# Optimization experiments

Measured on AMD Instinct MI355X. Metric: run time of the kernel, lower is better.

Reference implementation:

```python
import jax, jax.numpy as jnp
import numpy as np
from jax import lax

B, NPG = 128, 1024          # graphs, nodes per graph
N = B * NPG                  # total nodes
AVG_DEG = 8
E = N * AVG_DEG              # total edges
F_N, F_E = 128, 32           # node / edge feature dims
LATENT = [32, 32, 32, 1]
D = sum(LATENT)              # total_latent_dim = 97
K = 30                       # sort-pooling k
C1, C2, KW2 = 16, 32, 5      # conv1d channels / kernel
OUT = 2
DENSE = ((K - 2) // 2 + 1 - KW2 + 1) * C2  # 352


def setup_inputs() -> dict:
    key = jax.random.key(0)
    ks = jax.random.split(key, 12)
    inp = {}
    inp["node_feat"] = jax.random.normal(ks[0], (N, F_N), jnp.float32)
    inp["edge_feat"] = jax.random.normal(ks[1], (E, F_E), jnp.float32)
    inp["edge_index"] = jax.random.randint(ks[2], (2, E), 0, N)
    dims = [F_N + F_E] + LATENT
    for i in range(4):
        inp[f"W{i}"] = jax.random.normal(ks[3 + i], (dims[i], dims[i + 1]), jnp.float32) * 0.05
        inp[f"b{i}"] = jnp.zeros((dims[i + 1],), jnp.float32)
    inp["w_conv1"] = jax.random.normal(ks[7], (C1, 1, D), jnp.float32) * 0.05
    inp["b_conv1"] = jnp.zeros((C1,), jnp.float32)
    inp["w_conv2"] = jax.random.normal(ks[8], (C2, C1, KW2), jnp.float32) * 0.05
    inp["b_conv2"] = jnp.zeros((C2,), jnp.float32)
    inp["w_out"] = jax.random.normal(ks[9], (DENSE, OUT), jnp.float32) * 0.05
    inp["b_out"] = jnp.zeros((OUT,), jnp.float32)
    return inp


def _maxpool2(x):
    # MaxPool1d(2, 2) over last axis of [B, C, L]
    return lax.reduce_window(x, -jnp.inf, lax.max, (1, 1, 2), (1, 1, 2), "VALID")


def _forward(node_feat, edge_feat, W0, b0, W1, b1, W2, b2, W3, b3,
             w_conv1, b_conv1, w_conv2, b_conv2, w_out, b_out, edge_index):
    src, dst = edge_index[0], edge_index[1]
    # degree with self-loop, as in DGCNN (divide by deg after linear)
    deg = jnp.ones((N,), node_feat.dtype).at[dst].add(1.0)
    # e2npool: sum incident edge features onto destination nodes
    e2n = jax.ops.segment_sum(edge_feat, dst, num_segments=N)
    cur = jnp.concatenate([node_feat, e2n], axis=1)  # [N, F_N+F_E]
    hops = []
    for W, b in ((W0, b0), (W1, b1), (W2, b2), (W3, b3)):
        # (A + I) X  -> Linear -> / deg -> tanh
        pooled = jax.ops.segment_sum(cur[src], dst, num_segments=N) + cur
        cur = jnp.tanh((pooled @ W + b) / deg[:, None])
        hops.append(cur)
    feat = jnp.concatenate(hops, axis=1).reshape(B, NPG, D)  # [B, NPG, 97]
    # SortPooling: top-k nodes per graph by last latent channel
    _, idx = lax.top_k(feat[:, :, -1], K)                    # [B, K]
    sp = jnp.take_along_axis(feat, idx[:, :, None], axis=1)  # [B, K, D]
    x = sp.reshape(B, 1, K * D)
    x = lax.conv_general_dilated(x, w_conv1, (D,), "VALID",
                                 dimension_numbers=("NCH", "OIH", "NCH"))
    x = jax.nn.relu(x + b_conv1[None, :, None])  # [B, 16, 30]
    x = _maxpool2(x)                              # [B, 16, 15]
    x = lax.conv_general_dilated(x, w_conv2, (1,), "VALID",
                                 dimension_numbers=("NCH", "OIH", "NCH"))
    x = jax.nn.relu(x + b_conv2[None, :, None])  # [B, 32, 11]
    x = x.reshape(B, -1)                          # [B, 352]
    return jax.nn.relu(x @ w_out + b_out)         # [B, OUT]


def reference(node_feat, edge_feat, edge_index, W0, b0, W1, b1, W2, b2, W3, b3,
              w_conv1, b_conv1, w_conv2, b_conv2, w_out, b_out):
    return _forward(node_feat, edge_feat, W0, b0, W1, b1, W2, b2, W3, b3,
                    w_conv1, b_conv1, w_conv2, b_conv2, w_out, b_out, edge_index)
```

## Files before the change

kernel.cpp:

```cpp
#include <hip/hip_runtime.h>
#include <hip/hip_bf16.h>
#include <math.h>

#define N_NODES 131072
#define N_EDGES 1048576
#define B_GR    128
#define NPG_    1024
#define KTOP    30


__global__ __launch_bounds__(256) void k_zero(int* cnt) {
    int i = blockIdx.x * 256 + threadIdx.x;
    if (i < N_NODES) cnt[i] = 0;
}

__global__ __launch_bounds__(256) void k_count(const int* __restrict__ dst, int* __restrict__ cnt) {
    int xcd = blockIdx.x & 7;
    int base = (blockIdx.x >> 3) * 4096 + threadIdx.x;
    #pragma unroll
    for (int it = 0; it < 16; ++it) {
        int e = base + it * 256;
        int d = __builtin_nontemporal_load(dst + e);
        if ((d >> 14) == xcd) atomicAdd(&cnt[d], 1);
    }
}

__global__ __launch_bounds__(256) void k_scan1(const int* __restrict__ cnt,
                                               int* __restrict__ row_start,
                                               int* __restrict__ blocksum) {
    __shared__ int s[256];
    int t = threadIdx.x;
    int i = blockIdx.x * 256 + t;
    int v = cnt[i];
    s[t] = v; __syncthreads();
    for (int o = 1; o < 256; o <<= 1) {
        int x = (t >= o) ? s[t - o] : 0;
        __syncthreads();
        s[t] += x;
        __syncthreads();
    }
    row_start[i] = s[t] - v;
    if (t == 255) blocksum[blockIdx.x] = s[t];
}

__global__ __launch_bounds__(512) void k_scan2(int* __restrict__ blocksum) {
    __shared__ int s[512];
    int t = threadIdx.x;
    int v = blocksum[t];
    s[t] = v; __syncthreads();
    for (int o = 1; o < 512; o <<= 1) {
        int x = (t >= o) ? s[t - o] : 0;
        __syncthreads();
        s[t] += x;
        __syncthreads();
    }
    blocksum[t] = s[t] - v;
}

__global__ __launch_bounds__(256) void k_scan3(int* __restrict__ row_start,
                                               const int* __restrict__ blocksum,
                                               int* __restrict__ cursor) {
    int i = blockIdx.x * 256 + threadIdx.x;
    int r = row_start[i] + blocksum[blockIdx.x];
    row_start[i] = r;
    cursor[i] = r;
}

__global__ __launch_bounds__(256) void k_fill(const int* __restrict__ src,
                                              const int* __restrict__ dst,
                                              int* __restrict__ cursor,
                                              int* __restrict__ csr_src,
                                              int* __restrict__ csr_eid) {
    int xcd = blockIdx.x & 7;
    int base = (blockIdx.x >> 3) * 4096 + threadIdx.x;
    #pragma unroll
    for (int it = 0; it < 16; ++it) {
        int e = base + it * 256;
        int d = __builtin_nontemporal_load(dst + e);
        if ((d >> 14) == xcd) {
            int s = __builtin_nontemporal_load(src + e);
            int pos = atomicAdd(&cursor[d], 1);
            csr_src[pos] = s;
            csr_eid[pos] = e;
        }
    }
}


__global__ __launch_bounds__(256) void k_esum(const float* __restrict__ ef,
                                              const int* __restrict__ row_start,
                                              const int* __restrict__ cnt,
                                              const int* __restrict__ csr_eid,
                                              float* __restrict__ esum) {
    int g = threadIdx.x >> 5, j = threadIdx.x & 31;
    int n0 = (blockIdx.x * 8 + g) * 4;
    int st[4], ln[4];
    #pragma unroll
    for (int i = 0; i < 4; ++i) { st[i] = row_start[n0 + i]; ln[i] = cnt[n0 + i]; }
    float acc[4] = {0.f, 0.f, 0.f, 0.f};
    int base = 0;
    while ((ln[0] > base) | (ln[1] > base) | (ln[2] > base) | (ln[3] > base)) {
        int eid[4][8];
        #pragma unroll
        for (int i = 0; i < 4; ++i) {
            #pragma unroll
            for (int s = 0; s < 8; ++s) {
                int idx = base + s;
                int a = st[i] + ((idx < ln[i]) ? idx : 0);
                a = (a < N_EDGES) ? a : 0;
                eid[i][s] = csr_eid[a];
            }
        }
        #pragma unroll
        for (int i = 0; i < 4; ++i) {
            #pragma unroll
            for (int s = 0; s < 8; ++s) {
                float v = ef[(size_t)eid[i][s] * 32 + j];
                acc[i] += ((base + s) < ln[i]) ? v : 0.f;
            }
        }
        base += 8;
    }
    #pragma unroll
    for (int i = 0; i < 4; ++i)
        esum[(size_t)(n0 + i) * 32 + j] = acc[i];
}


__global__ __launch_bounds__(256) void k_gemm160(const float* __restrict__ nf,
                                                 const float* __restrict__ esum,
                                                 const float* __restrict__ W0,
                                                 float* __restrict__ z0) {
    __shared__ float a[64 * 161];
    int tid = threadIdx.x;
    int n0 = blockIdx.x * 64;
    const float* nfb = nf + (size_t)n0 * 128;
    for (int f = tid; f < 8192; f += 256) {
        int n = f >> 7, k = f & 127;
        a[n * 161 + k] = nfb[f];
    }
    const float* esb = esum + (size_t)n0 * 32;
    for (int f = tid; f < 2048; f += 256) {
        int n = f >> 5, k = f & 31;
        a[n * 161 + 128 + k] = esb[f];
    }
    __syncthreads();
    int wv = __builtin_amdgcn_readfirstlane(tid >> 6);
    int lane = tid & 63;
    int c0 = wv * 8;
    float acc[8] = {0.f, 0.f, 0.f, 0.f, 0.f, 0.f, 0.f, 0.f};
    const float* ar = a + lane * 161;
    for (int k = 0; k < 160; ++k) {
        float av = ar[k];
        #pragma unroll
        for (int jj = 0; jj < 8; ++jj)
            acc[jj] += av * W0[k * 32 + c0 + jj];
    }
    float* zr = z0 + (size_t)(n0 + lane) * 32 + c0;
    *(float4*)zr = make_float4(acc[0], acc[1], acc[2], acc[3]);
    *(float4*)(zr + 4) = make_float4(acc[4], acc[5], acc[6], acc[7]);
}


__global__ __launch_bounds__(256) void k_layer(const float* __restrict__ zin,
                                               const int* __restrict__ row_start,
                                               const int* __restrict__ cnt,
                                               const int* __restrict__ csr_src,
                                               const float* __restrict__ bias,
                                               const float* __restrict__ Wn,
                                               float* __restrict__ hout,
                                               float* __restrict__ znext) {
    __shared__ float Ws[1024];
    int tid = threadIdx.x;
    for (int f = tid; f < 1024; f += 256) Ws[f] = Wn[f];
    __syncthreads();
    int g = tid >> 5, j = tid & 31;
    int n0 = (blockIdx.x * 8 + g) * 4;
    int st[4], ln[4];
    #pragma unroll
    for (int i = 0; i < 4; ++i) { st[i] = row_start[n0 + i]; ln[i] = cnt[n0 + i]; }
    float acc[4];
    #pragma unroll
    for (int i = 0; i < 4; ++i) acc[i] = zin[(size_t)(n0 + i) * 32 + j];
    int base = 0;
    while ((ln[0] > base) | (ln[1] > base) | (ln[2] > base) | (ln[3] > base)) {
        int sid[4][8];
        #pragma unroll
        for (int i = 0; i < 4; ++i) {
            #pragma unroll
            for (int s = 0; s < 8; ++s) {
                int idx = base + s;
                int a = st[i] + ((idx < ln[i]) ? idx : 0);
                a = (a < N_EDGES) ? a : 0;
                sid[i][s] = csr_src[a];
            }
        }
        #pragma unroll
        for (int i = 0; i < 4; ++i) {
            #pragma unroll
            for (int s = 0; s < 8; ++s) {
                float v = zin[(size_t)sid[i][s] * 32 + j];
                acc[i] += ((base + s) < ln[i]) ? v : 0.f;
            }
        }
        base += 8;
    }
    float bj = bias[j];
    float h[4];
    #pragma unroll
    for (int i = 0; i < 4; ++i) {
        float deg = 1.f + (float)ln[i];
        h[i] = tanhf((acc[i] + bj) / deg);
        hout[(size_t)(n0 + i) * 32 + j] = h[i];
    }
    float z[4] = {0.f, 0.f, 0.f, 0.f};
    for (int k = 0; k < 32; ++k) {
        float w = Ws[k * 32 + j];
        #pragma unroll
        for (int i = 0; i < 4; ++i)
            z[i] += __shfl(h[i], k, 32) * w;
    }
    #pragma unroll
    for (int i = 0; i < 4; ++i)
        znext[(size_t)(n0 + i) * 32 + j] = z[i];
}


__global__ __launch_bounds__(256) void k_layer3(const float* __restrict__ zin,
                                                const int* __restrict__ row_start,
                                                const int* __restrict__ cnt,
                                                const int* __restrict__ csr_src,
                                                const float* __restrict__ bias,
                                                const float* __restrict__ W3,
                                                float* __restrict__ hout,
                                                float* __restrict__ z3) {
    int g = threadIdx.x >> 5, j = threadIdx.x & 31;
    int n0 = (blockIdx.x * 8 + g) * 4;
    int st[4], ln[4];
    #pragma unroll
    for (int i = 0; i < 4; ++i) { st[i] = row_start[n0 + i]; ln[i] = cnt[n0 + i]; }
    float acc[4];
    #pragma unroll
    for (int i = 0; i < 4; ++i) acc[i] = zin[(size_t)(n0 + i) * 32 + j];
    int base = 0;
    while ((ln[0] > base) | (ln[1] > base) | (ln[2] > base) | (ln[3] > base)) {
        int sid[4][8];
        #pragma unroll
        for (int i = 0; i < 4; ++i) {
            #pragma unroll
            for (int s = 0; s < 8; ++s) {
                int idx = base + s;
                int a = st[i] + ((idx < ln[i]) ? idx : 0);
                a = (a < N_EDGES) ? a : 0;
                sid[i][s] = csr_src[a];
            }
        }
        #pragma unroll
        for (int i = 0; i < 4; ++i) {
            #pragma unroll
            for (int s = 0; s < 8; ++s) {
                float v = zin[(size_t)sid[i][s] * 32 + j];
                acc[i] += ((base + s) < ln[i]) ? v : 0.f;
            }
        }
        base += 8;
    }
    float bj = bias[j];
    float w3 = W3[j];
    #pragma unroll
    for (int i = 0; i < 4; ++i) {
        float deg = 1.f + (float)ln[i];
        float h = tanhf((acc[i] + bj) / deg);
        hout[(size_t)(n0 + i) * 32 + j] = h;
        float t = h * w3;
        #pragma unroll
        for (int o = 16; o; o >>= 1) t += __shfl_xor(t, o, 32);
        if (j == 0) z3[n0 + i] = t;
    }
}


__global__ __launch_bounds__(256) void k_g3(const float* __restrict__ z3,
                                            const int* __restrict__ row_start,
                                            const int* __restrict__ cnt,
                                            const int* __restrict__ csr_src,
                                            const float* __restrict__ b3,
                                            float* __restrict__ val) {
    int n = blockIdx.x * 256 + threadIdx.x;
    int start = row_start[n], len = cnt[n];
    const int* cs = csr_src + start;
    float s = z3[n];
    int i = 0;
    for (; i + 4 <= len; i += 4)
        s += z3[cs[i]] + z3[cs[i + 1]] + z3[cs[i + 2]] + z3[cs[i + 3]];
    for (; i < len; ++i) s += z3[cs[i]];
    float deg = 1.f + (float)len;
    val[n] = tanhf((s + b3[0]) / deg);
}


__global__ __launch_bounds__(256) void k_head(const float* __restrict__ h0,
                                              const float* __restrict__ h1,
                                              const float* __restrict__ h2,
                                              const float* __restrict__ val,
                                              const float* __restrict__ wc1,
                                              const float* __restrict__ bc1,
                                              const float* __restrict__ wc2,
                                              const float* __restrict__ bc2,
                                              const float* __restrict__ wout,
                                              const float* __restrict__ bout,
                                              float* __restrict__ out) {
    __shared__ float vals[1024];
    __shared__ int selidx[KTOP];
    __shared__ float sp[KTOP * 97];
    __shared__ float y1[16 * 30];
    __shared__ float pool[16 * 15];
    __shared__ float y2[352];
    int b = blockIdx.x, tid = threadIdx.x;
    const float* vb = val + (size_t)b * NPG_;
    for (int u = tid; u < NPG_; u += 256) vals[u] = vb[u];
    __syncthreads();
    if (tid < 64) {
        unsigned long long keys[16];
        #pragma unroll
        for (int r = 0; r < 16; ++r) {
            int u = tid * 16 + r;
            unsigned int bb = __float_as_uint(vals[u]);
            unsigned int ord = (bb & 0x80000000u) ? ~bb : (bb | 0x80000000u);
            keys[r] = ((unsigned long long)ord << 32) |
                      (unsigned long long)(0xFFFFFFFFu - (unsigned int)u);
        }
        for (int k = 0; k < KTOP; ++k) {
            unsigned long long m = keys[0];
            #pragma unroll
            for (int r = 1; r < 16; ++r) m = (keys[r] > m) ? keys[r] : m;
            #pragma unroll
            for (int o = 32; o; o >>= 1) {
                unsigned long long t = __shfl_xor(m, o);
                m = (t > m) ? t : m;
            }
            int u = (int)(0xFFFFFFFFu - (unsigned int)(m & 0xFFFFFFFFull));
            if (tid == 0) selidx[k] = u;
            #pragma unroll
            for (int r = 0; r < 16; ++r)
                if (tid * 16 + r == u) keys[r] = 0ull;
        }
    }
    __syncthreads();
    size_t nb = (size_t)b * NPG_;
    for (int idx = tid; idx < KTOP * 32; idx += 256) {
        int t = idx >> 5, d = idx & 31;
        size_t s = (nb + (size_t)selidx[t]) * 32;
        sp[t * 97 + d]      = h0[s + d];
        sp[t * 97 + 32 + d] = h1[s + d];
        sp[t * 97 + 64 + d] = h2[s + d];
    }
    if (tid < KTOP) sp[tid * 97 + 96] = vb[selidx[tid]];
    __syncthreads();
    for (int idx = tid; idx < 480; idx += 256) {
        int t = idx >> 4, c = idx & 15;
        float acc = bc1[c];
        for (int d = 0; d < 97; ++d) acc += sp[t * 97 + d] * wc1[c * 97 + d];
        y1[c * 30 + t] = fmaxf(acc, 0.f);
    }
    __syncthreads();
    for (int idx = tid; idx < 240; idx += 256) {
        int c = idx / 15, u = idx - c * 15;
        pool[c * 15 + u] = fmaxf(y1[c * 30 + 2 * u], y1[c * 30 + 2 * u + 1]);
    }
    __syncthreads();
    for (int idx = tid; idx < 352; idx += 256) {
        int o = idx / 11, t = idx - o * 11;
        float acc = bc2[o];
        for (int i = 0; i < 16; ++i)
            for (int kk = 0; kk < 5; ++kk)
                acc += pool[i * 15 + t + kk] * wc2[(o * 16 + i) * 5 + kk];
        y2[idx] = fmaxf(acc, 0.f);
    }
    __syncthreads();
    if (tid < 2) {
        float acc = bout[tid];
        for (int m = 0; m < 352; ++m) acc += y2[m] * wout[m * 2 + tid];
        out[b * 2 + tid] = fmaxf(acc, 0.f);
    }
}


extern "C" void kernel_launch(void* const* d_in, const int* in_sizes, int n_in,
                              void* d_out, int out_size, void* d_ws, size_t ws_size,
                              hipStream_t stream) {
    const float* node_feat = (const float*)d_in[0];
    const float* edge_feat = (const float*)d_in[1];
    const int*   eidx      = (const int*)d_in[2];
    const float* W0 = (const float*)d_in[3];
    const float* b0 = (const float*)d_in[4];
    const float* W1 = (const float*)d_in[5];
    const float* b1 = (const float*)d_in[6];
    const float* W2 = (const float*)d_in[7];
    const float* b2 = (const float*)d_in[8];
    const float* W3 = (const float*)d_in[9];
    const float* b3 = (const float*)d_in[10];
    const float* wc1 = (const float*)d_in[11];
    const float* bc1 = (const float*)d_in[12];
    const float* wc2 = (const float*)d_in[13];
    const float* bc2 = (const float*)d_in[14];
    const float* wout = (const float*)d_in[15];
    const float* bout = (const float*)d_in[16];
    float* out = (float*)d_out;

    const int* src = eidx;
    const int* dst = eidx + N_EDGES;

    char* ws = (char*)d_ws;
    size_t off = 0;
    auto alloc = [&](size_t bytes) -> char* {
        char* p = ws + off;
        off += (bytes + 255) & ~(size_t)255;
        return p;
    };
    int* cnt       = (int*)alloc((size_t)N_NODES * 4);
    int* row_start = (int*)alloc((size_t)N_NODES * 4);
    int* cursor    = (int*)alloc((size_t)N_NODES * 4);
    int* blocksum  = (int*)alloc(512 * 4);
    int* csr_src   = (int*)alloc((size_t)N_EDGES * 4);
    int* csr_eid   = (int*)alloc((size_t)N_EDGES * 4);
    float* esum    = (float*)alloc((size_t)N_NODES * 32 * 4);
    float* z0      = (float*)alloc((size_t)N_NODES * 32 * 4);
    float* z1      = (float*)alloc((size_t)N_NODES * 32 * 4);
    float* z2      = (float*)alloc((size_t)N_NODES * 32 * 4);
    float* h0      = (float*)alloc((size_t)N_NODES * 32 * 4);
    float* h1      = (float*)alloc((size_t)N_NODES * 32 * 4);
    float* h2      = (float*)alloc((size_t)N_NODES * 32 * 4);
    float* z3      = (float*)alloc((size_t)N_NODES * 4);
    float* val     = (float*)alloc((size_t)N_NODES * 4);
    (void)ws_size;

    k_zero<<<N_NODES / 256, 256, 0, stream>>>(cnt);
    k_count<<<2048, 256, 0, stream>>>(dst, cnt);
    k_scan1<<<N_NODES / 256, 256, 0, stream>>>(cnt, row_start, blocksum);
    k_scan2<<<1, 512, 0, stream>>>(blocksum);
    k_scan3<<<N_NODES / 256, 256, 0, stream>>>(row_start, blocksum, cursor);
    k_fill<<<2048, 256, 0, stream>>>(src, dst, cursor, csr_src, csr_eid);
    k_esum<<<N_NODES / 32, 256, 0, stream>>>(edge_feat, row_start, cnt, csr_eid, esum);
    k_gemm160<<<N_NODES / 64, 256, 0, stream>>>(node_feat, esum, W0, z0);
    k_layer<<<N_NODES / 32, 256, 0, stream>>>(z0, row_start, cnt, csr_src, b0, W1, h0, z1);
    k_layer<<<N_NODES / 32, 256, 0, stream>>>(z1, row_start, cnt, csr_src, b1, W2, h1, z2);
    k_layer3<<<N_NODES / 32, 256, 0, stream>>>(z2, row_start, cnt, csr_src, b2, W3, h2, z3);
    k_g3<<<N_NODES / 256, 256, 0, stream>>>(z3, row_start, cnt, csr_src, b3, val);
    k_head<<<B_GR, 256, 0, stream>>>(h0, h1, h2, val, wc1, bc1, wc2, bc2, wout, bout, out);
}
```

Before: 582.2 us.

## Fuse edge-sum into first GEMM and restructure layers to aggregate then transform

Edge-feature segment sum moves into the first GEMM kernel, which writes directly into its shared-memory tile, so the separate esum kernel and its global round trip go away. The layer kernels now aggregate h and then apply the 32x32 weight in the same kernel, instead of precomputing z for the next layer. This removes the z1/z2 buffers and their writes. The zeroing kernel is replaced by hipMemsetAsync. A risk is that the GEMM kernel now does the irregular gather with 8 nodes per group, which may lower occupancy or add load imbalance before the tile math.

```diff
diff --git a/kernel.cpp b/kernel.cpp
--- a/kernel.cpp
+++ b/kernel.cpp
@@ -8,11 +8,6 @@
 #define NPG_    1024
 #define KTOP    30
 
-
-__global__ __launch_bounds__(256) void k_zero(int* cnt) {
-    int i = blockIdx.x * 256 + threadIdx.x;
-    if (i < N_NODES) cnt[i] = 0;
-}
 
 __global__ __launch_bounds__(256) void k_count(const int* __restrict__ dst, int* __restrict__ cnt) {
     int xcd = blockIdx.x & 7;
@@ -87,48 +82,11 @@
 }
 
 
-__global__ __launch_bounds__(256) void k_esum(const float* __restrict__ ef,
-                                              const int* __restrict__ row_start,
-                                              const int* __restrict__ cnt,
-                                              const int* __restrict__ csr_eid,
-                                              float* __restrict__ esum) {
-    int g = threadIdx.x >> 5, j = threadIdx.x & 31;
-    int n0 = (blockIdx.x * 8 + g) * 4;
-    int st[4], ln[4];
-    #pragma unroll
-    for (int i = 0; i < 4; ++i) { st[i] = row_start[n0 + i]; ln[i] = cnt[n0 + i]; }
-    float acc[4] = {0.f, 0.f, 0.f, 0.f};
-    int base = 0;
-    while ((ln[0] > base) | (ln[1] > base) | (ln[2] > base) | (ln[3] > base)) {
-        int eid[4][8];
-        #pragma unroll
-        for (int i = 0; i < 4; ++i) {
-            #pragma unroll
-            for (int s = 0; s < 8; ++s) {
-                int idx = base + s;
-                int a = st[i] + ((idx < ln[i]) ? idx : 0);
-                a = (a < N_EDGES) ? a : 0;
-                eid[i][s] = csr_eid[a];
-            }
-        }
-        #pragma unroll
-        for (int i = 0; i < 4; ++i) {
-            #pragma unroll
-            for (int s = 0; s < 8; ++s) {
-                float v = ef[(size_t)eid[i][s] * 32 + j];
-                acc[i] += ((base + s) < ln[i]) ? v : 0.f;
-            }
-        }
-        base += 8;
-    }
-    #pragma unroll
-    for (int i = 0; i < 4; ++i)
-        esum[(size_t)(n0 + i) * 32 + j] = acc[i];
-}
-
-
 __global__ __launch_bounds__(256) void k_gemm160(const float* __restrict__ nf,
-                                                 const float* __restrict__ esum,
+                                                 const float* __restrict__ ef,
+                                                 const int* __restrict__ row_start,
+                                                 const int* __restrict__ cnt,
+                                                 const int* __restrict__ csr_eid,
                                                  const float* __restrict__ W0,
                                                  float* __restrict__ z0) {
     __shared__ float a[64 * 161];
@@ -139,42 +97,64 @@
         int n = f >> 7, k = f & 127;
         a[n * 161 + k] = nfb[f];
     }
-    const float* esb = esum + (size_t)n0 * 32;
-    for (int f = tid; f < 2048; f += 256) {
-        int n = f >> 5, k = f & 31;
-        a[n * 161 + 128 + k] = esb[f];
-    }
+    int g = tid >> 5, j = tid & 31;
+    int nb = n0 + g * 8;
+    int st[8], ln[8];
+    #pragma unroll
+    for (int i = 0; i < 8; ++i) { st[i] = row_start[nb + i]; ln[i] = cnt[nb + i]; }
+    int mx = 0;
+    #pragma unroll
+    for (int i = 0; i < 8; ++i) mx = max(mx, ln[i]);
+    float acc[8] = {0.f, 0.f, 0.f, 0.f, 0.f, 0.f, 0.f, 0.f};
+    for (int base = 0; base < mx; base += 8) {
+        int eid[8][8];
+        #pragma unroll
+        for (int i = 0; i < 8; ++i) {
+            #pragma unroll
+            for (int s = 0; s < 8; ++s) {
+                int idx = base + s;
+                int ad = st[i] + ((idx < ln[i]) ? idx : 0);
+                ad = (ad < N_EDGES) ? ad : 0;
+                eid[i][s] = csr_eid[ad];
+            }
+        }
+        #pragma unroll
+        for (int i = 0; i < 8; ++i) {
+            #pragma unroll
+            for (int s = 0; s < 8; ++s) {
+                float v = ef[(size_t)eid[i][s] * 32 + j];
+                acc[i] += ((base + s) < ln[i]) ? v : 0.f;
+            }
+        }
+    }
+    #pragma unroll
+    for (int i = 0; i < 8; ++i)
+        a[(g * 8 + i) * 161 + 128 + j] = acc[i];
     __syncthreads();
     int wv = __builtin_amdgcn_readfirstlane(tid >> 6);
     int lane = tid & 63;
     int c0 = wv * 8;
-    float acc[8] = {0.f, 0.f, 0.f, 0.f, 0.f, 0.f, 0.f, 0.f};
+    float o[8] = {0.f, 0.f, 0.f, 0.f, 0.f, 0.f, 0.f, 0.f};
     const float* ar = a + lane * 161;
     for (int k = 0; k < 160; ++k) {
         float av = ar[k];
         #pragma unroll
         for (int jj = 0; jj < 8; ++jj)
-            acc[jj] += av * W0[k * 32 + c0 + jj];
+            o[jj] += av * W0[k * 32 + c0 + jj];
     }
     float* zr = z0 + (size_t)(n0 + lane) * 32 + c0;
-    *(float4*)zr = make_float4(acc[0], acc[1], acc[2], acc[3]);
-    *(float4*)(zr + 4) = make_float4(acc[4], acc[5], acc[6], acc[7]);
-}
-
-
-__global__ __launch_bounds__(256) void k_layer(const float* __restrict__ zin,
-                                               const int* __restrict__ row_start,
-                                               const int* __restrict__ cnt,
-                                               const int* __restrict__ csr_src,
-                                               const float* __restrict__ bias,
-                                               const float* __restrict__ Wn,
-                                               float* __restrict__ hout,
-                                               float* __restrict__ znext) {
-    __shared__ float Ws[1024];
-    int tid = threadIdx.x;
-    for (int f = tid; f < 1024; f += 256) Ws[f] = Wn[f];
-    __syncthreads();
-    int g = tid >> 5, j = tid & 31;
+    *(float4*)zr = make_float4(o[0], o[1], o[2], o[3]);
+    *(float4*)(zr + 4) = make_float4(o[4], o[5], o[6], o[7]);
+}
+
+
+__global__ __launch_bounds__(256) void k_layerA(const float* __restrict__ zin,
+                                                const int* __restrict__ row_start,
+                                                const int* __restrict__ cnt,
+                                                const int* __restrict__ csr_src,
+                                                const float* __restrict__ bias,
+                                                float* __restrict__ hout) {
+    int g = threadIdx.x >> 5, j = threadIdx.x & 31;
     int n0 = (blockIdx.x * 8 + g) * 4;
     int st[4], ln[4];
     #pragma unroll
@@ -190,9 +170,9 @@
             #pragma unroll
             for (int s = 0; s < 8; ++s) {
                 int idx = base + s;
-                int a = st[i] + ((idx < ln[i]) ? idx : 0);
-                a = (a < N_EDGES) ? a : 0;
-                sid[i][s] = csr_src[a];
+                int ad = st[i] + ((idx < ln[i]) ? idx : 0);
+                ad = (ad < N_EDGES) ? ad : 0;
+                sid[i][s] = csr_src[ad];
             }
         }
         #pragma unroll
@@ -206,42 +186,89 @@
         base += 8;
     }
     float bj = bias[j];
-    float h[4];
-    #pragma unroll
-    for (int i = 0; i < 4; ++i) {
-        float deg = 1.f + (float)ln[i];
-        h[i] = tanhf((acc[i] + bj) / deg);
-        hout[(size_t)(n0 + i) * 32 + j] = h[i];
-    }
-    float z[4] = {0.f, 0.f, 0.f, 0.f};
-    for (int k = 0; k < 32; ++k) {
-        float w = Ws[k * 32 + j];
-        #pragma unroll
-        for (int i = 0; i < 4; ++i)
-            z[i] += __shfl(h[i], k, 32) * w;
-    }
     #pragma unroll
     for (int i = 0; i < 4; ++i)
-        znext[(size_t)(n0 + i) * 32 + j] = z[i];
-}
-
-
-__global__ __launch_bounds__(256) void k_layer3(const float* __restrict__ zin,
+        hout[(size_t)(n0 + i) * 32 + j] = tanhf((acc[i] + bj) / (1.f + (float)ln[i]));
+}
+
+
+__global__ __launch_bounds__(256) void k_layerB(const float* __restrict__ hin,
                                                 const int* __restrict__ row_start,
                                                 const int* __restrict__ cnt,
                                                 const int* __restrict__ csr_src,
                                                 const float* __restrict__ bias,
+                                                const float* __restrict__ Wn,
+                                                float* __restrict__ hout) {
+    __shared__ float Ws[1024];
+    int tid = threadIdx.x;
+    for (int f = tid; f < 1024; f += 256) Ws[f] = Wn[f];
+    __syncthreads();
+    int g = tid >> 5, j = tid & 31;
+    int n0 = (blockIdx.x * 8 + g) * 4;
+    int st[4], ln[4];
+    #pragma unroll
+    for (int i = 0; i < 4; ++i) { st[i] = row_start[n0 + i]; ln[i] = cnt[n0 + i]; }
+    float acc[4];
+    #pragma unroll
+    for (int i = 0; i < 4; ++i) acc[i] = hin[(size_t)(n0 + i) * 32 + j];
+    int base = 0;
+    while ((ln[0] > base) | (ln[1] > base) | (ln[2] > base) | (ln[3] > base)) {
+        int sid[4][8];
+        #pragma unroll
+        for (int i = 0; i < 4; ++i) {
+            #pragma unroll
+            for (int s = 0; s < 8; ++s) {
+                int idx = base + s;
+                int ad = st[i] + ((idx < ln[i]) ? idx : 0);
+                ad = (ad < N_EDGES) ? ad : 0;
+                sid[i][s] = csr_src[ad];
+            }
+        }
+        #pragma unroll
+        for (int i = 0; i < 4; ++i) {
+            #pragma unroll
+            for (int s = 0; s < 8; ++s) {
+                float v = hin[(size_t)sid[i][s] * 32 + j];
+                acc[i] += ((base + s) < ln[i]) ? v : 0.f;
+            }
+        }
+        base += 8;
+    }
+    float y[4] = {0.f, 0.f, 0.f, 0.f};
+    for (int k = 0; k < 32; ++k) {
+        float w = Ws[k * 32 + j];
+        #pragma unroll
+        for (int i = 0; i < 4; ++i)
+            y[i] += __shfl(acc[i], k, 32) * w;
+    }
+    float bj = bias[j];
+    #pragma unroll
+    for (int i = 0; i < 4; ++i)
+        hout[(size_t)(n0 + i) * 32 + j] = tanhf((y[i] + bj) / (1.f + (float)ln[i]));
+}
+
+
+__global__ __launch_bounds__(256) void k_layerC(const float* __restrict__ hin,
+                                                const int* __restrict__ row_start,
+                                                const int* __restrict__ cnt,
+                                                const int* __restrict__ csr_src,
+                                                const float* __restrict__ bias,
+                                                const float* __restrict__ Wn,
                                                 const float* __restrict__ W3,
                                                 float* __restrict__ hout,
                                                 float* __restrict__ z3) {
-    int g = threadIdx.x >> 5, j = threadIdx.x & 31;
+    __shared__ float Ws[1024];
+    int tid = threadIdx.x;
+    for (int f = tid; f < 1024; f += 256) Ws[f] = Wn[f];
+    __syncthreads();
+    int g = tid >> 5, j = tid & 31;
     int n0 = (blockIdx.x * 8 + g) * 4;
     int st[4], ln[4];
     #pragma unroll
     for (int i = 0; i < 4; ++i) { st[i] = row_start[n0 + i]; ln[i] = cnt[n0 + i]; }
     float acc[4];
     #pragma unroll
-    for (int i = 0; i < 4; ++i) acc[i] = zin[(size_t)(n0 + i) * 32 + j];
+    for (int i = 0; i < 4; ++i) acc[i] = hin[(size_t)(n0 + i) * 32 + j];
     int base = 0;
     while ((ln[0] > base) | (ln[1] > base) | (ln[2] > base) | (ln[3] > base)) {
         int sid[4][8];
@@ -250,27 +277,33 @@
             #pragma unroll
             for (int s = 0; s < 8; ++s) {
                 int idx = base + s;
-                int a = st[i] + ((idx < ln[i]) ? idx : 0);
-                a = (a < N_EDGES) ? a : 0;
-                sid[i][s] = csr_src[a];
-            }
-        }
-        #pragma unroll
-        for (int i = 0; i < 4; ++i) {
-            #pragma unroll
-            for (int s = 0; s < 8; ++s) {
-                float v = zin[(size_t)sid[i][s] * 32 + j];
+                int ad = st[i] + ((idx < ln[i]) ? idx : 0);
+                ad = (ad < N_EDGES) ? ad : 0;
+                sid[i][s] = csr_src[ad];
+            }
+        }
+        #pragma unroll
+        for (int i = 0; i < 4; ++i) {
+            #pragma unroll
+            for (int s = 0; s < 8; ++s) {
+                float v = hin[(size_t)sid[i][s] * 32 + j];
                 acc[i] += ((base + s) < ln[i]) ? v : 0.f;
             }
         }
         base += 8;
+    }
+    float y[4] = {0.f, 0.f, 0.f, 0.f};
+    for (int k = 0; k < 32; ++k) {
+        float w = Ws[k * 32 + j];
+        #pragma unroll
+        for (int i = 0; i < 4; ++i)
+            y[i] += __shfl(acc[i], k, 32) * w;
     }
     float bj = bias[j];
     float w3 = W3[j];
     #pragma unroll
     for (int i = 0; i < 4; ++i) {
-        float deg = 1.f + (float)ln[i];
-        float h = tanhf((acc[i] + bj) / deg);
+        float h = tanhf((y[i] + bj) / (1.f + (float)ln[i]));
         hout[(size_t)(n0 + i) * 32 + j] = h;
         float t = h * w3;
         #pragma unroll
@@ -424,10 +457,7 @@
     int* blocksum  = (int*)alloc(512 * 4);
     int* csr_src   = (int*)alloc((size_t)N_EDGES * 4);
     int* csr_eid   = (int*)alloc((size_t)N_EDGES * 4);
-    float* esum    = (float*)alloc((size_t)N_NODES * 32 * 4);
     float* z0      = (float*)alloc((size_t)N_NODES * 32 * 4);
-    float* z1      = (float*)alloc((size_t)N_NODES * 32 * 4);
-    float* z2      = (float*)alloc((size_t)N_NODES * 32 * 4);
     float* h0      = (float*)alloc((size_t)N_NODES * 32 * 4);
     float* h1      = (float*)alloc((size_t)N_NODES * 32 * 4);
     float* h2      = (float*)alloc((size_t)N_NODES * 32 * 4);
@@ -435,17 +465,17 @@
     float* val     = (float*)alloc((size_t)N_NODES * 4);
     (void)ws_size;
 
-    k_zero<<<N_NODES / 256, 256, 0, stream>>>(cnt);
+    hipMemsetAsync(cnt, 0, (size_t)N_NODES * 4, stream);
     k_count<<<2048, 256, 0, stream>>>(dst, cnt);
     k_scan1<<<N_NODES / 256, 256, 0, stream>>>(cnt, row_start, blocksum);
     k_scan2<<<1, 512, 0, stream>>>(blocksum);
     k_scan3<<<N_NODES / 256, 256, 0, stream>>>(row_start, blocksum, cursor);
     k_fill<<<2048, 256, 0, stream>>>(src, dst, cursor, csr_src, csr_eid);
-    k_esum<<<N_NODES / 32, 256, 0, stream>>>(edge_feat, row_start, cnt, csr_eid, esum);
-    k_gemm160<<<N_NODES / 64, 256, 0, stream>>>(node_feat, esum, W0, z0);
-    k_layer<<<N_NODES / 32, 256, 0, stream>>>(z0, row_start, cnt, csr_src, b0, W1, h0, z1);
-    k_layer<<<N_NODES / 32, 256, 0, stream>>>(z1, row_start, cnt, csr_src, b1, W2, h1, z2);
-    k_layer3<<<N_NODES / 32, 256, 0, stream>>>(z2, row_start, cnt, csr_src, b2, W3, h2, z3);
+    k_gemm160<<<N_NODES / 64, 256, 0, stream>>>(node_feat, edge_feat, row_start, cnt,
+                                                csr_eid, W0, z0);
+    k_layerA<<<N_NODES / 32, 256, 0, stream>>>(z0, row_start, cnt, csr_src, b0, h0);
+    k_layerB<<<N_NODES / 32, 256, 0, stream>>>(h0, row_start, cnt, csr_src, b1, W1, h1);
+    k_layerC<<<N_NODES / 32, 256, 0, stream>>>(h1, row_start, cnt, csr_src, b2, W2, W3, h2, z3);
     k_g3<<<N_NODES / 256, 256, 0, stream>>>(z3, row_start, cnt, csr_src, b3, val);
     k_head<<<B_GR, 256, 0, stream>>>(h0, h1, h2, val, wc1, bc1, wc2, bc2, wout, bout, out);
 }
```

Result: slower. 627.5 us (+7.8%).
